# Kernel optimization log

Measured on AMD Instinct MI355X. Metric: run time of the kernel, lower is better.

The kernel has to match this reference:

```python
import jax, jax.numpy as jnp
import numpy as np

NUM_LAYERS = 4
HIDDEN = 512
HEADS = 8
DK = HIDDEN // HEADS
REPR_IN = 53
REPR_HID = 32
LN_EPS = 1e-5


def _mask_by_1dmask(x, mask):
    # x: [B,H,L,L], mask: [B,L] bool
    pair = mask[:, :, None] & mask[:, None, :]          # [B,L,L]
    masked = jnp.where(pair[:, None, :, :], x, -jnp.inf)
    all_inf = jnp.all(masked == -jnp.inf, axis=-1, keepdims=True)
    return jnp.where(all_inf, 0.0, masked)


def _layernorm(x, g, b):
    mu = jnp.mean(x, axis=-1, keepdims=True)
    var = jnp.mean((x - mu) ** 2, axis=-1, keepdims=True)
    return (x - mu) * jax.lax.rsqrt(var + LN_EPS) * g + b


def _attn_block(x, mask, refCov, Wq, bq, Wk, bk, Wv, bv, Wo, bo,
                Wr1, br1, Wr2, br2, ln_g, ln_b):
    B, L, h = x.shape
    residual = x
    q = (x @ Wq + bq).reshape(B, L, HEADS, DK).transpose(0, 2, 1, 3)  # [B,H,L,dk]
    k = (x @ Wk + bk).reshape(B, L, HEADS, DK).transpose(0, 2, 1, 3)
    v = (x @ Wv + bv).reshape(B, L, HEADS, DK).transpose(0, 2, 1, 3)
    scores = jnp.einsum('bhid,bhjd->bhij', q, k) / np.sqrt(DK).astype(np.float32)
    scores = _mask_by_1dmask(scores, mask)
    attn_w = jax.nn.softmax(scores, axis=-1)
    # per-pair MLP bias: [B,L,L,53] -> [B,L,L,H] -> [B,H,L,L]
    ref = jax.nn.relu(refCov @ Wr1 + br1) @ Wr2 + br2
    ref = ref.transpose(0, 3, 1, 2)
    ref = _mask_by_1dmask(ref, mask)
    ref_w = jax.nn.softmax(ref, axis=-1)
    comb = attn_w + ref_w
    comb = comb / jnp.sum(comb, axis=-1, keepdims=True)
    out = jnp.einsum('bhij,bhjd->bhid', comb, v)
    out = out.transpose(0, 2, 1, 3).reshape(B, L, h)
    out = out @ Wo + bo
    return _layernorm(residual + out, ln_g, ln_b)


def setup_inputs() -> dict:
    key = jax.random.key(0)
    ks = jax.random.split(key, 20)
    B, L = 8, 384
    s = 0.02
    inp = {
        'x': jax.random.normal(ks[0], (B, L, HIDDEN), jnp.float32),
        'mask': jax.random.randint(ks[1], (B, L), 0, 2) > 0,
        'refCov': jax.random.normal(ks[2], (B, L, L, REPR_IN), jnp.float32),
        'Wq': jax.random.normal(ks[3], (NUM_LAYERS, HIDDEN, HIDDEN)) * s,
        'bq': jnp.zeros((NUM_LAYERS, HIDDEN)),
        'Wk': jax.random.normal(ks[4], (NUM_LAYERS, HIDDEN, HIDDEN)) * s,
        'bk': jnp.zeros((NUM_LAYERS, HIDDEN)),
        'Wv': jax.random.normal(ks[5], (NUM_LAYERS, HIDDEN, HIDDEN)) * s,
        'bv': jnp.zeros((NUM_LAYERS, HIDDEN)),
        'Wo': jax.random.normal(ks[6], (NUM_LAYERS, HIDDEN, HIDDEN)) * s,
        'bo': jnp.zeros((NUM_LAYERS, HIDDEN)),
        'Wr1': jax.random.normal(ks[7], (NUM_LAYERS, REPR_IN, REPR_HID)) * 0.1,
        'br1': jnp.zeros((NUM_LAYERS, REPR_HID)),
        'Wr2': jax.random.normal(ks[8], (NUM_LAYERS, REPR_HID, HEADS)) * 0.1,
        'br2': jnp.zeros((NUM_LAYERS, HEADS)),
        'ln_g': jnp.ones((NUM_LAYERS, HIDDEN)),
        'ln_b': jnp.zeros((NUM_LAYERS, HIDDEN)),
        'fn_g': jnp.ones((HIDDEN,)),
        'fn_b': jnp.zeros((HIDDEN,)),
    }
    return inp


def reference(x, mask, refCov, Wq, bq, Wk, bk, Wv, bv, Wo, bo,
              Wr1, br1, Wr2, br2, ln_g, ln_b, fn_g, fn_b):
    # process_node_feature packs flat nodes into [B,L,h] with zeros at padding;
    # equivalent here to zeroing padded positions of x.
    h = x * mask[:, :, None].astype(x.dtype)
    for i in range(NUM_LAYERS):
        h = _attn_block(h, mask, refCov, Wq[i], bq[i], Wk[i], bk[i],
                        Wv[i], bv[i], Wo[i], bo[i], Wr1[i], br1[i],
                        Wr2[i], br2[i], ln_g[i], ln_b[i])
    h = _layernorm(h, fn_g, fn_b)
    return jnp.sum(h * mask[:, :, None].astype(h.dtype), axis=1)  # [B, HIDDEN]
```

## Files before the change

kernel.cpp:

```cpp
#include <hip/hip_runtime.h>
#include <hip/hip_bf16.h>
#include <cstdint>

constexpr int LSEQ  = 384;
constexpr int BATCH = 8;
constexpr int HID   = 512;
constexpr int NHEAD = 8;
constexpr int DKH   = 64;
constexpr int NLAY  = 4;
constexpr int BL    = BATCH * LSEQ;
constexpr int LL2   = LSEQ * LSEQ;
constexpr int BH    = BATCH * NHEAD;

typedef __bf16 bf16x8 __attribute__((ext_vector_type(8)));
typedef float  f32x4  __attribute__((ext_vector_type(4)));
typedef unsigned short ushort_t;

__device__ inline bf16x8 load_frag(const void* p) {
    uint4 u = *reinterpret_cast<const uint4*>(p);
    return __builtin_bit_cast(bf16x8, u);
}
__device__ inline bf16x8 zero_frag() {
    uint4 u = {0u, 0u, 0u, 0u};
    return __builtin_bit_cast(bf16x8, u);
}
__device__ inline f32x4 mfma16(bf16x8 a, bf16x8 b, f32x4 c) {
    return __builtin_amdgcn_mfma_f32_16x16x32_bf16(a, b, c, 0, 0, 0);
}
__device__ inline float b2f(__hip_bfloat16 v) { return __bfloat162float(v); }
__device__ inline ushort_t bfbits(float f) {
    __hip_bfloat16 b = __float2bfloat16(f);
    return *(ushort_t*)&b;
}

__global__ __launch_bounds__(1024) void mask_norm_kernel(
    const unsigned char* __restrict__ raw, unsigned char* __restrict__ m)
{
    __shared__ int fl;
    const int tid = threadIdx.x;
    if (tid == 0) fl = 0;
    __syncthreads();
    int f = 0;
    for (int i = tid; i < BL; i += 1024) {
        const unsigned char v = raw[i];
        if (v > 1) f |= 1;
        if (v && (i & 3)) f |= 2;
        if (v && ((i & 7) == 4)) f |= 4;
        if (v && ((i & 3) <= 1)) f |= 8;
    }
    if (f) atomicOr(&fl, f);
    __syncthreads();
    const int ff = fl;
    int stride, off;
    if (ff & 1) { if (ff & 8) { stride = 2; off = 0; } else { stride = 4; off = 2; } }
    else if (ff & 2) { stride = 1; off = 0; }
    else if (ff & 4) { stride = 4; off = 0; }
    else             { stride = 8; off = 0; }
    for (int i = tid; i < BL; i += 1024)
        m[i] = raw[(size_t)i * stride + off] ? 1 : 0;
}

__global__ __launch_bounds__(256) void wconv_kernel(
    const float* __restrict__ Wq, const float* __restrict__ Wk,
    const float* __restrict__ Wv, const float* __restrict__ Wo,
    ushort_t* __restrict__ WTqkv, ushort_t* __restrict__ WTo)
{
    __shared__ float tile[32][33];
    const int t = blockIdx.x;
    const int ml = t >> 8;
    const int rest = t & 255;
    const int mi = ml >> 2, l = ml & 3;
    const int tk = (rest & 15) * 32;
    const int tn = (rest >> 4) * 32;
    const float* W = (mi == 0) ? Wq : (mi == 1) ? Wk : (mi == 2) ? Wv : Wo;
    const float* src = W + (size_t)l * HID * HID;
    const int c = threadIdx.x & 31, r = threadIdx.x >> 5;
    for (int rr = r; rr < 32; rr += 8)
        tile[rr][c] = src[(size_t)(tk + rr) * HID + tn + c];
    __syncthreads();
    ushort_t* dst = (mi < 3)
        ? WTqkv + ((size_t)l * 1536 + mi * 512) * HID
        : WTo   + (size_t)l * HID * HID;
    for (int rr = r; rr < 32; rr += 8)
        dst[(size_t)(tn + rr) * HID + tk + c] = bfbits(tile[c][rr]);
}

__global__ __launch_bounds__(256) void refw_kernel(
    const float* __restrict__ Wr1, const float* __restrict__ Wr2,
    ushort_t* __restrict__ W1T, ushort_t* __restrict__ W2T)
{
    const int tid = blockIdx.x * 256 + threadIdx.x;
    if (tid < 4 * 32 * 64) {
        const int l = tid >> 11, rem = tid & 2047;
        const int n = rem >> 6, k = rem & 63;
        W1T[tid] = (k < 53) ? bfbits(Wr1[(l * 53 + k) * 32 + n]) : (ushort_t)0;
    } else if (tid < 4 * 32 * 64 + 4 * 16 * 32) {
        const int t2 = tid - 8192;
        const int l = t2 >> 9, rem = t2 & 511;
        const int n = rem >> 5, k = rem & 31;
        W2T[t2] = (n < 8) ? bfbits(Wr2[(l * 32 + k) * 8 + n]) : (ushort_t)0;
    }
}

__global__ __launch_bounds__(256) void pack_kernel(
    const float* __restrict__ x, const unsigned char* __restrict__ mask,
    float* __restrict__ h, __hip_bfloat16* __restrict__ hb)
{
    const int idx = blockIdx.x * 256 + threadIdx.x;
    const int row = idx >> 9;
    const float v = mask[row] ? x[idx] : 0.f;
    h[idx] = v;
    hb[idx] = __float2bfloat16(v);
}

__global__ __launch_bounds__(256) void refmlp_kernel(
    const float* __restrict__ refCov,
    const ushort_t* __restrict__ W1T, const float* __restrict__ br1,
    const ushort_t* __restrict__ W2T, const float* __restrict__ br2,
    __hip_bfloat16* __restrict__ refL)
{
    __shared__ ushort_t smem[256 * 56];

    const int tid = threadIdx.x;
    const int w = tid >> 6, lane = tid & 63;
    const int lr = lane & 15, quad = lane >> 4;
    const size_t p0 = (size_t)blockIdx.x * 256;
    const int b = (int)(p0 / LL2);
    const int rem0 = (int)(p0 - (size_t)b * LL2);

    const float4* src4 = reinterpret_cast<const float4*>(refCov + p0 * 53);
    for (int f = tid; f < 3392; f += 256) {
        float4 v = src4[f];
        const int e = f * 4;
        #pragma unroll
        for (int k = 0; k < 4; ++k) {
            const int g = e + k;
            const int row = g / 53;
            const int col = g - row * 53;
            smem[row * 56 + col] = bfbits(((const float*)&v)[k]);
        }
    }
    smem[tid * 56 + 53] = 0;
    smem[tid * 56 + 54] = 0;
    smem[tid * 56 + 55] = 0;
    __syncthreads();

    bf16x8 afr[4][2];
    #pragma unroll
    for (int mi = 0; mi < 4; ++mi) {
        const ushort_t* rp = smem + (w * 64 + mi * 16 + lr) * 56;
        afr[mi][0] = load_frag(rp + quad * 8);
        afr[mi][1] = (quad < 3) ? load_frag(rp + 32 + quad * 8) : zero_frag();
    }
    __syncthreads();

    ushort_t* C1w = smem + w * 2560;

    #pragma unroll
    for (int l = 0; l < NLAY; ++l) {
        const float bias0 = br1[l * 32 + lr];
        const float bias1 = br1[l * 32 + 16 + lr];
        const float bias2 = br2[l * 8 + (lr & 7)];
        bf16x8 w1f[2][2];
        #pragma unroll
        for (int ni = 0; ni < 2; ++ni)
            #pragma unroll
            for (int ks = 0; ks < 2; ++ks)
                w1f[ni][ks] = load_frag(W1T + ((l * 32 + ni * 16 + lr) * 64) + ks * 32 + quad * 8);
        bf16x8 w2f = load_frag(W2T + (l * 16 + lr) * 32 + quad * 8);

        f32x4 acc[4][2];
        #pragma unroll
        for (int mi = 0; mi < 4; ++mi) {
            acc[mi][0] = (f32x4){bias0, bias0, bias0, bias0};
            acc[mi][1] = (f32x4){bias1, bias1, bias1, bias1};
        }
        #pragma unroll
        for (int mi = 0; mi < 4; ++mi) {
            acc[mi][0] = mfma16(afr[mi][0], w1f[0][0], acc[mi][0]);
            acc[mi][0] = mfma16(afr[mi][1], w1f[0][1], acc[mi][0]);
            acc[mi][1] = mfma16(afr[mi][0], w1f[1][0], acc[mi][1]);
            acc[mi][1] = mfma16(afr[mi][1], w1f[1][1], acc[mi][1]);
        }
        #pragma unroll
        for (int mi = 0; mi < 4; ++mi)
            #pragma unroll
            for (int ni = 0; ni < 2; ++ni)
                #pragma unroll
                for (int r = 0; r < 4; ++r)
                    C1w[(mi * 16 + quad * 4 + r) * 40 + ni * 16 + lr] =
                        bfbits(fmaxf(acc[mi][ni][r], 0.f));

        #pragma unroll
        for (int mi = 0; mi < 4; ++mi) {
            bf16x8 a2 = load_frag(C1w + (mi * 16 + lr) * 40 + quad * 8);
            f32x4 a = (f32x4){bias2, bias2, bias2, bias2};
            a = mfma16(a2, w2f, a);
            if (lr < 8) {
                uint2 pk;
                pk.x = (unsigned)bfbits(a[0]) | ((unsigned)bfbits(a[1]) << 16);
                pk.y = (unsigned)bfbits(a[2]) | ((unsigned)bfbits(a[3]) << 16);
                const size_t plane = ((size_t)(l * 8 + b) * 8 + lr) * LL2;
                *reinterpret_cast<uint2*>((ushort_t*)refL + plane + rem0 +
                                          w * 64 + mi * 16 + quad * 4) = pk;
            }
        }
    }
}

__global__ __launch_bounds__(256) void gemm_qkv_kernel(
    const __hip_bfloat16* __restrict__ A,
    const __hip_bfloat16* __restrict__ BT,
    const float* __restrict__ bq, const float* __restrict__ bk,
    const float* __restrict__ bv,
    __hip_bfloat16* __restrict__ q, __hip_bfloat16* __restrict__ kk,
    __hip_bfloat16* __restrict__ vT)
{
    const int bm = blockIdx.x % (BL / 64);
    const int bn = blockIdx.x / (BL / 64);
    const int wv = threadIdx.x >> 6;
    const int lane = threadIdx.x & 63;
    const int lr = lane & 15, quad = lane >> 4;
    const int m0 = bm * 64 + (wv & 1) * 32;
    const int n0g = bn * 64 + (wv >> 1) * 32;
    f32x4 acc[2][2];
    #pragma unroll
    for (int i = 0; i < 2; ++i)
        #pragma unroll
        for (int j = 0; j < 2; ++j) acc[i][j] = (f32x4){0.f, 0.f, 0.f, 0.f};
    const __hip_bfloat16* a0p = A + (size_t)(m0 + lr) * HID;
    const __hip_bfloat16* a1p = A + (size_t)(m0 + 16 + lr) * HID;
    const __hip_bfloat16* b0p = BT + (size_t)(n0g + lr) * HID;
    const __hip_bfloat16* b1p = BT + (size_t)(n0g + 16 + lr) * HID;
    #pragma unroll 4
    for (int k0 = 0; k0 < HID; k0 += 32) {
        const int ka = k0 + quad * 8;
        bf16x8 a0 = load_frag(a0p + ka);
        bf16x8 a1 = load_frag(a1p + ka);
        bf16x8 b0 = load_frag(b0p + ka);
        bf16x8 b1 = load_frag(b1p + ka);
        acc[0][0] = mfma16(a0, b0, acc[0][0]);
        acc[0][1] = mfma16(a0, b1, acc[0][1]);
        acc[1][0] = mfma16(a1, b0, acc[1][0]);
        acc[1][1] = mfma16(a1, b1, acc[1][1]);
    }
    const int mat = n0g >> 9;
    const float* bias = (mat == 0) ? bq : (mat == 1) ? bk : bv;
    const float scale = (mat == 0) ? 0.125f : 1.0f;
    __hip_bfloat16* outp = (mat == 0) ? q : (mat == 1) ? kk : vT;
    #pragma unroll
    for (int mi = 0; mi < 2; ++mi)
        #pragma unroll
        for (int ni = 0; ni < 2; ++ni)
            #pragma unroll
            for (int r = 0; r < 4; ++r) {
                const int m = m0 + mi * 16 + quad * 4 + r;
                const int ng = n0g + ni * 16 + lr;
                const int n = ng & 511;
                float v = (acc[mi][ni][r] + bias[n]) * scale;
                const int bb = m / LSEQ, ii = m % LSEQ;
                const int hh = n >> 6, d = n & 63;
                if (mat == 2)
                    outp[((size_t)(bb * NHEAD + hh) * DKH + d) * LSEQ + ii] = __float2bfloat16(v);
                else
                    outp[((size_t)(bb * NHEAD + hh) * LSEQ + ii) * DKH + d] = __float2bfloat16(v);
            }
}

__global__ __launch_bounds__(256) void gemm_oproj_kernel(
    const __hip_bfloat16* __restrict__ A,
    const __hip_bfloat16* __restrict__ BT,
    const float* __restrict__ bias,
    float* __restrict__ outf)
{
    const int bm = blockIdx.x % (BL / 64);
    const int bn = blockIdx.x / (BL / 64);
    const int wv = threadIdx.x >> 6;
    const int lane = threadIdx.x & 63;
    const int lr = lane & 15, quad = lane >> 4;
    const int m0 = bm * 64 + (wv & 1) * 32;
    const int n0 = bn * 64 + (wv >> 1) * 32;
    f32x4 acc[2][2];
    #pragma unroll
    for (int i = 0; i < 2; ++i)
        #pragma unroll
        for (int j = 0; j < 2; ++j) acc[i][j] = (f32x4){0.f, 0.f, 0.f, 0.f};
    const __hip_bfloat16* a0p = A + (size_t)(m0 + lr) * HID;
    const __hip_bfloat16* a1p = A + (size_t)(m0 + 16 + lr) * HID;
    const __hip_bfloat16* b0p = BT + (size_t)(n0 + lr) * HID;
    const __hip_bfloat16* b1p = BT + (size_t)(n0 + 16 + lr) * HID;
    #pragma unroll 4
    for (int k0 = 0; k0 < HID; k0 += 32) {
        const int ka = k0 + quad * 8;
        bf16x8 a0 = load_frag(a0p + ka);
        bf16x8 a1 = load_frag(a1p + ka);
        bf16x8 b0 = load_frag(b0p + ka);
        bf16x8 b1 = load_frag(b1p + ka);
        acc[0][0] = mfma16(a0, b0, acc[0][0]);
        acc[0][1] = mfma16(a0, b1, acc[0][1]);
        acc[1][0] = mfma16(a1, b0, acc[1][0]);
        acc[1][1] = mfma16(a1, b1, acc[1][1]);
    }
    #pragma unroll
    for (int mi = 0; mi < 2; ++mi)
        #pragma unroll
        for (int ni = 0; ni < 2; ++ni)
            #pragma unroll
            for (int r = 0; r < 4; ++r) {
                const int m = m0 + mi * 16 + quad * 4 + r;
                const int n = n0 + ni * 16 + lr;
                outf[(size_t)m * HID + n] = acc[mi][ni][r] + bias[n];
            }
}

__global__ __launch_bounds__(256) void gemm_scores_kernel(
    const __hip_bfloat16* __restrict__ Q,
    const __hip_bfloat16* __restrict__ Km,
    float* __restrict__ S)
{
    const int bh = blockIdx.x / 36;
    const int t = blockIdx.x % 36;
    const int bm = t % 6, bn = t / 6;
    const int wv = threadIdx.x >> 6;
    const int lane = threadIdx.x & 63;
    const int lr = lane & 15, quad = lane >> 4;
    const int m0 = bm * 64 + (wv & 1) * 32;
    const int n0 = bn * 64 + (wv >> 1) * 32;
    const __hip_bfloat16* qb = Q + (size_t)bh * LSEQ * DKH;
    const __hip_bfloat16* kb = Km + (size_t)bh * LSEQ * DKH;
    f32x4 acc[2][2];
    #pragma unroll
    for (int i = 0; i < 2; ++i)
        #pragma unroll
        for (int j = 0; j < 2; ++j) acc[i][j] = (f32x4){0.f, 0.f, 0.f, 0.f};
    #pragma unroll
    for (int k0 = 0; k0 < DKH; k0 += 32) {
        const int ka = k0 + quad * 8;
        bf16x8 a0 = load_frag(qb + (size_t)(m0 + lr) * DKH + ka);
        bf16x8 a1 = load_frag(qb + (size_t)(m0 + 16 + lr) * DKH + ka);
        bf16x8 b0 = load_frag(kb + (size_t)(n0 + lr) * DKH + ka);
        bf16x8 b1 = load_frag(kb + (size_t)(n0 + 16 + lr) * DKH + ka);
        acc[0][0] = mfma16(a0, b0, acc[0][0]);
        acc[0][1] = mfma16(a0, b1, acc[0][1]);
        acc[1][0] = mfma16(a1, b0, acc[1][0]);
        acc[1][1] = mfma16(a1, b1, acc[1][1]);
    }
    float* srow = S + (size_t)bh * LL2;
    #pragma unroll
    for (int mi = 0; mi < 2; ++mi)
        #pragma unroll
        for (int ni = 0; ni < 2; ++ni)
            #pragma unroll
            for (int r = 0; r < 4; ++r) {
                const int m = m0 + mi * 16 + quad * 4 + r;
                const int n = n0 + ni * 16 + lr;
                srow[(size_t)m * LSEQ + n] = acc[mi][ni][r];
            }
}

__global__ __launch_bounds__(256) void softmax_comb_kernel(
    const float* __restrict__ S, const __hip_bfloat16* __restrict__ refl,
    const unsigned char* __restrict__ mask, __hip_bfloat16* __restrict__ comb)
{
    const int wv = threadIdx.x >> 6, lane = threadIdx.x & 63;
    const int row = blockIdx.x * 4 + wv;
    const int bh = row / LSEQ, i = row % LSEQ;
    const int b = bh >> 3;
    const size_t roff = (size_t)row * LSEQ;
    __hip_bfloat16* crow = comb + roff;
    if (!mask[b * LSEQ + i]) {
        const __hip_bfloat16 z = __float2bfloat16(0.f);
        #pragma unroll
        for (int t = 0; t < 6; ++t) crow[lane + 64 * t] = z;
        return;
    }
    const float* srow = S + roff;
    const __hip_bfloat16* rrow = refl + roff;
    float sv[6], rv[6];
    #pragma unroll
    for (int t = 0; t < 6; ++t) {
        const int j = lane + 64 * t;
        const bool vm = mask[b * LSEQ + j] != 0;
        sv[t] = vm ? srow[j] : -1e30f;
        rv[t] = vm ? b2f(rrow[j]) : -1e30f;
    }
    float ms = -1e30f, mr = -1e30f;
    #pragma unroll
    for (int t = 0; t < 6; ++t) { ms = fmaxf(ms, sv[t]); mr = fmaxf(mr, rv[t]); }
    #pragma unroll
    for (int off = 32; off > 0; off >>= 1) {
        ms = fmaxf(ms, __shfl_xor(ms, off));
        mr = fmaxf(mr, __shfl_xor(mr, off));
    }
    float es[6], er[6], Ss = 0.f, Sr = 0.f;
    #pragma unroll
    for (int t = 0; t < 6; ++t) {
        es[t] = __expf(sv[t] - ms); Ss += es[t];
        er[t] = __expf(rv[t] - mr); Sr += er[t];
    }
    #pragma unroll
    for (int off = 32; off > 0; off >>= 1) {
        Ss += __shfl_xor(Ss, off);
        Sr += __shfl_xor(Sr, off);
    }
    const float cs = 0.5f / Ss, cr = 0.5f / Sr;
    #pragma unroll
    for (int t = 0; t < 6; ++t)
        crow[lane + 64 * t] = __float2bfloat16(es[t] * cs + er[t] * cr);
}

__global__ __launch_bounds__(256) void gemm_out_kernel(
    const __hip_bfloat16* __restrict__ C,
    const __hip_bfloat16* __restrict__ VT,
    __hip_bfloat16* __restrict__ AO)
{
    const int bh = blockIdx.x / 6;
    const int bm = blockIdx.x % 6;
    const int wv = threadIdx.x >> 6;
    const int lane = threadIdx.x & 63;
    const int lr = lane & 15, quad = lane >> 4;
    const int m0 = bm * 64 + (wv & 1) * 32;
    const int n0 = (wv >> 1) * 32;
    const __hip_bfloat16* cb = C + (size_t)bh * LL2;
    const __hip_bfloat16* vb = VT + (size_t)bh * DKH * LSEQ;
    f32x4 acc[2][2];
    #pragma unroll
    for (int i = 0; i < 2; ++i)
        #pragma unroll
        for (int j = 0; j < 2; ++j) acc[i][j] = (f32x4){0.f, 0.f, 0.f, 0.f};
    #pragma unroll 4
    for (int k0 = 0; k0 < LSEQ; k0 += 32) {
        const int ka = k0 + quad * 8;
        bf16x8 a0 = load_frag(cb + (size_t)(m0 + lr) * LSEQ + ka);
        bf16x8 a1 = load_frag(cb + (size_t)(m0 + 16 + lr) * LSEQ + ka);
        bf16x8 b0 = load_frag(vb + (size_t)(n0 + lr) * LSEQ + ka);
        bf16x8 b1 = load_frag(vb + (size_t)(n0 + 16 + lr) * LSEQ + ka);
        acc[0][0] = mfma16(a0, b0, acc[0][0]);
        acc[0][1] = mfma16(a0, b1, acc[0][1]);
        acc[1][0] = mfma16(a1, b0, acc[1][0]);
        acc[1][1] = mfma16(a1, b1, acc[1][1]);
    }
    const int bb = bh >> 3, hh = bh & 7;
    #pragma unroll
    for (int mi = 0; mi < 2; ++mi)
        #pragma unroll
        for (int ni = 0; ni < 2; ++ni)
            #pragma unroll
            for (int r = 0; r < 4; ++r) {
                const int m = m0 + mi * 16 + quad * 4 + r;
                const int n = n0 + ni * 16 + lr;
                AO[(size_t)(bb * LSEQ + m) * HID + hh * DKH + n] =
                    __float2bfloat16(acc[mi][ni][r]);
            }
}

__global__ __launch_bounds__(256) void ln_kernel(
    const float* __restrict__ resid, const float* __restrict__ proj,
    const float* __restrict__ g, const float* __restrict__ beta,
    float* __restrict__ outf, __hip_bfloat16* __restrict__ outb,
    const unsigned char* __restrict__ mask, int flags)
{
    const int row = blockIdx.x, tid = threadIdx.x;
    const size_t base = (size_t)row * HID;
    float x0 = resid[base + tid], x1 = resid[base + tid + 256];
    if (flags & 1) { x0 += proj[base + tid]; x1 += proj[base + tid + 256]; }
    float s = x0 + x1, s2 = x0 * x0 + x1 * x1;
    #pragma unroll
    for (int off = 32; off > 0; off >>= 1) {
        s += __shfl_xor(s, off);
        s2 += __shfl_xor(s2, off);
    }
    __shared__ float rs[4], rs2[4];
    if ((tid & 63) == 0) { rs[tid >> 6] = s; rs2[tid >> 6] = s2; }
    __syncthreads();
    s = rs[0] + rs[1] + rs[2] + rs[3];
    s2 = rs2[0] + rs2[1] + rs2[2] + rs2[3];
    const float mu = s * (1.f / HID);
    const float var = s2 * (1.f / HID) - mu * mu;
    const float rstd = rsqrtf(var + 1e-5f);
    float y0 = (x0 - mu) * rstd * g[tid] + beta[tid];
    float y1 = (x1 - mu) * rstd * g[tid + 256] + beta[tid + 256];
    if ((flags & 2) && !mask[row]) { y0 = 0.f; y1 = 0.f; }
    outf[base + tid] = y0;
    outf[base + tid + 256] = y1;
    if (flags & 4) {
        outb[base + tid] = __float2bfloat16(y0);
        outb[base + tid + 256] = __float2bfloat16(y1);
    }
}

__global__ __launch_bounds__(512) void reduce_kernel(
    const float* __restrict__ hf, float* __restrict__ out)
{
    const int b = blockIdx.x, c = threadIdx.x;
    float s = 0.f;
    for (int i = 0; i < LSEQ; ++i)
        s += hf[((size_t)(b * LSEQ + i)) * HID + c];
    out[b * HID + c] = s;
}

extern "C" void kernel_launch(void* const* d_in, const int* in_sizes, int n_in,
                              void* d_out, int out_size, void* d_ws, size_t ws_size,
                              hipStream_t stream)
{
    const float* x   = (const float*)d_in[0];
    const unsigned char* mraw = (const unsigned char*)d_in[1];
    const float* refCov = (const float*)d_in[2];
    const float* Wq = (const float*)d_in[3];
    const float* bq = (const float*)d_in[4];
    const float* Wk = (const float*)d_in[5];
    const float* bk = (const float*)d_in[6];
    const float* Wv = (const float*)d_in[7];
    const float* bv = (const float*)d_in[8];
    const float* Wo = (const float*)d_in[9];
    const float* bo = (const float*)d_in[10];
    const float* Wr1 = (const float*)d_in[11];
    const float* br1 = (const float*)d_in[12];
    const float* Wr2 = (const float*)d_in[13];
    const float* br2 = (const float*)d_in[14];
    const float* ln_g = (const float*)d_in[15];
    const float* ln_b = (const float*)d_in[16];
    const float* fn_g = (const float*)d_in[17];
    const float* fn_b = (const float*)d_in[18];
    float* outp = (float*)d_out;

    char* ws = (char*)d_ws;
    size_t off = 0;
    auto alloc = [&](size_t bytes) -> char* {
        char* p = ws + off;
        off += (bytes + 255) & ~(size_t)255;
        return p;
    };
    __hip_bfloat16* refL  = (__hip_bfloat16*)alloc((size_t)NLAY * BH * LL2 * 2);
    float*          h     = (float*)alloc((size_t)BL * HID * 4);
    __hip_bfloat16* hb    = (__hip_bfloat16*)alloc((size_t)BL * HID * 2);
    __hip_bfloat16* q     = (__hip_bfloat16*)alloc((size_t)BH * LSEQ * DKH * 2);
    __hip_bfloat16* kk    = (__hip_bfloat16*)alloc((size_t)BH * LSEQ * DKH * 2);
    __hip_bfloat16* vT    = (__hip_bfloat16*)alloc((size_t)BH * DKH * LSEQ * 2);
    float*          S     = (float*)alloc((size_t)BH * LL2 * 4);
    __hip_bfloat16* comb  = (__hip_bfloat16*)alloc((size_t)BH * LL2 * 2);
    __hip_bfloat16* AO    = (__hip_bfloat16*)alloc((size_t)BL * HID * 2);
    float*          proj  = (float*)alloc((size_t)BL * HID * 4);
    ushort_t*       WTqkv = (ushort_t*)alloc((size_t)NLAY * 1536 * HID * 2);
    ushort_t*       WTo   = (ushort_t*)alloc((size_t)NLAY * HID * HID * 2);
    ushort_t*       W1T   = (ushort_t*)alloc((size_t)4 * 32 * 64 * 2);
    ushort_t*       W2T   = (ushort_t*)alloc((size_t)4 * 16 * 32 * 2);
    unsigned char*  msk   = (unsigned char*)alloc(BL);
    float*          hfin  = S;

    mask_norm_kernel<<<1, 1024, 0, stream>>>(mraw, msk);
    wconv_kernel<<<4096, 256, 0, stream>>>(Wq, Wk, Wv, Wo, WTqkv, WTo);
    refw_kernel<<<40, 256, 0, stream>>>(Wr1, Wr2, W1T, W2T);
    pack_kernel<<<6144, 256, 0, stream>>>(x, msk, h, hb);
    refmlp_kernel<<<4608, 256, 0, stream>>>(refCov, W1T, br1, W2T, br2, refL);

    for (int l = 0; l < NLAY; ++l) {
        const __hip_bfloat16* WTl = (const __hip_bfloat16*)(WTqkv + (size_t)l * 1536 * HID);
        const __hip_bfloat16* WTol = (const __hip_bfloat16*)(WTo + (size_t)l * HID * HID);
        gemm_qkv_kernel<<<1152, 256, 0, stream>>>(hb, WTl, bq + l * HID, bk + l * HID,
                                                  bv + l * HID, q, kk, vT);
        gemm_scores_kernel<<<2304, 256, 0, stream>>>(q, kk, S);
        softmax_comb_kernel<<<6144, 256, 0, stream>>>(S, refL + (size_t)l * BH * LL2, msk, comb);
        gemm_out_kernel<<<384, 256, 0, stream>>>(comb, vT, AO);
        gemm_oproj_kernel<<<384, 256, 0, stream>>>(AO, WTol, bo + l * HID, proj);
        ln_kernel<<<3072, 256, 0, stream>>>(h, proj, ln_g + l * HID, ln_b + l * HID,
                                            h, hb, nullptr, 1 | 4);
    }
    ln_kernel<<<3072, 256, 0, stream>>>(h, nullptr, fn_g, fn_b, hfin, nullptr, msk, 2);
    reduce_kernel<<<8, 512, 0, stream>>>(hfin, outp);
}
```

Baseline: 907.6 us.

## Fuse scores, dual softmax and PV matmul into one attention kernel

Replaces the three per-layer kernels (QK^T scores to fp32 global, softmax combine to bf16 global, comb@V) with one kernel per 32-row tile of each batch-head. Scores are kept in registers, the row max and sum are reduced across wavefronts through shared memory, and the combined probabilities are written to LDS and fed straight into the PV MFMA. This removes the round trips of the full fp32 scores and bf16 comb tensors through HBM plus two launches per layer. The cost is more registers per thread, a 25KB LDS tile, and only 768 blocks, which may lower occupancy.

```diff
diff --git a/kernel.cpp b/kernel.cpp
--- a/kernel.cpp
+++ b/kernel.cpp
@@ -313,145 +313,149 @@
             }
 }
 
-__global__ __launch_bounds__(256) void gemm_scores_kernel(
+__global__ __launch_bounds__(256) void attn_fused_kernel(
     const __hip_bfloat16* __restrict__ Q,
     const __hip_bfloat16* __restrict__ Km,
-    float* __restrict__ S)
-{
-    const int bh = blockIdx.x / 36;
-    const int t = blockIdx.x % 36;
-    const int bm = t % 6, bn = t / 6;
-    const int wv = threadIdx.x >> 6;
-    const int lane = threadIdx.x & 63;
+    const __hip_bfloat16* __restrict__ VT,
+    const __hip_bfloat16* __restrict__ refl,
+    const unsigned char* __restrict__ mask,
+    __hip_bfloat16* __restrict__ AO)
+{
+    __shared__ __align__(16) ushort_t Pl[32 * 392];
+    __shared__ float redm_s[2][2][16], redm_r[2][2][16];
+    __shared__ float reds_s[2][2][16], reds_r[2][2][16];
+
+    const int bh = blockIdx.x / 12;
+    const int i0 = (blockIdx.x % 12) * 32;
+    const int b  = bh >> 3, hh = bh & 7;
+    const int w = threadIdx.x >> 6, lane = threadIdx.x & 63;
+    const int s = w & 1, h2 = w >> 1;
     const int lr = lane & 15, quad = lane >> 4;
-    const int m0 = bm * 64 + (wv & 1) * 32;
-    const int n0 = bn * 64 + (wv >> 1) * 32;
-    const __hip_bfloat16* qb = Q + (size_t)bh * LSEQ * DKH;
+
+    const __hip_bfloat16* qb = Q  + (size_t)bh * LSEQ * DKH;
     const __hip_bfloat16* kb = Km + (size_t)bh * LSEQ * DKH;
-    f32x4 acc[2][2];
-    #pragma unroll
-    for (int i = 0; i < 2; ++i)
-        #pragma unroll
-        for (int j = 0; j < 2; ++j) acc[i][j] = (f32x4){0.f, 0.f, 0.f, 0.f};
+    const unsigned char* mrow = mask + b * LSEQ;
+
+    f32x4 acc[12];
+    #pragma unroll
+    for (int nt = 0; nt < 12; ++nt) acc[nt] = (f32x4){0.f, 0.f, 0.f, 0.f};
     #pragma unroll
     for (int k0 = 0; k0 < DKH; k0 += 32) {
         const int ka = k0 + quad * 8;
-        bf16x8 a0 = load_frag(qb + (size_t)(m0 + lr) * DKH + ka);
-        bf16x8 a1 = load_frag(qb + (size_t)(m0 + 16 + lr) * DKH + ka);
-        bf16x8 b0 = load_frag(kb + (size_t)(n0 + lr) * DKH + ka);
-        bf16x8 b1 = load_frag(kb + (size_t)(n0 + 16 + lr) * DKH + ka);
-        acc[0][0] = mfma16(a0, b0, acc[0][0]);
-        acc[0][1] = mfma16(a0, b1, acc[0][1]);
-        acc[1][0] = mfma16(a1, b0, acc[1][0]);
-        acc[1][1] = mfma16(a1, b1, acc[1][1]);
-    }
-    float* srow = S + (size_t)bh * LL2;
-    #pragma unroll
-    for (int mi = 0; mi < 2; ++mi)
-        #pragma unroll
-        for (int ni = 0; ni < 2; ++ni)
-            #pragma unroll
-            for (int r = 0; r < 4; ++r) {
-                const int m = m0 + mi * 16 + quad * 4 + r;
-                const int n = n0 + ni * 16 + lr;
-                srow[(size_t)m * LSEQ + n] = acc[mi][ni][r];
-            }
-}
-
-__global__ __launch_bounds__(256) void softmax_comb_kernel(
-    const float* __restrict__ S, const __hip_bfloat16* __restrict__ refl,
-    const unsigned char* __restrict__ mask, __hip_bfloat16* __restrict__ comb)
-{
-    const int wv = threadIdx.x >> 6, lane = threadIdx.x & 63;
-    const int row = blockIdx.x * 4 + wv;
-    const int bh = row / LSEQ, i = row % LSEQ;
-    const int b = bh >> 3;
-    const size_t roff = (size_t)row * LSEQ;
-    __hip_bfloat16* crow = comb + roff;
-    if (!mask[b * LSEQ + i]) {
-        const __hip_bfloat16 z = __float2bfloat16(0.f);
-        #pragma unroll
-        for (int t = 0; t < 6; ++t) crow[lane + 64 * t] = z;
-        return;
-    }
-    const float* srow = S + roff;
-    const __hip_bfloat16* rrow = refl + roff;
-    float sv[6], rv[6];
-    #pragma unroll
-    for (int t = 0; t < 6; ++t) {
-        const int j = lane + 64 * t;
-        const bool vm = mask[b * LSEQ + j] != 0;
-        sv[t] = vm ? srow[j] : -1e30f;
-        rv[t] = vm ? b2f(rrow[j]) : -1e30f;
-    }
-    float ms = -1e30f, mr = -1e30f;
-    #pragma unroll
-    for (int t = 0; t < 6; ++t) { ms = fmaxf(ms, sv[t]); mr = fmaxf(mr, rv[t]); }
-    #pragma unroll
-    for (int off = 32; off > 0; off >>= 1) {
-        ms = fmaxf(ms, __shfl_xor(ms, off));
-        mr = fmaxf(mr, __shfl_xor(mr, off));
-    }
-    float es[6], er[6], Ss = 0.f, Sr = 0.f;
-    #pragma unroll
-    for (int t = 0; t < 6; ++t) {
-        es[t] = __expf(sv[t] - ms); Ss += es[t];
-        er[t] = __expf(rv[t] - mr); Sr += er[t];
-    }
-    #pragma unroll
-    for (int off = 32; off > 0; off >>= 1) {
-        Ss += __shfl_xor(Ss, off);
-        Sr += __shfl_xor(Sr, off);
-    }
-    const float cs = 0.5f / Ss, cr = 0.5f / Sr;
-    #pragma unroll
-    for (int t = 0; t < 6; ++t)
-        crow[lane + 64 * t] = __float2bfloat16(es[t] * cs + er[t] * cr);
-}
-
-__global__ __launch_bounds__(256) void gemm_out_kernel(
-    const __hip_bfloat16* __restrict__ C,
-    const __hip_bfloat16* __restrict__ VT,
-    __hip_bfloat16* __restrict__ AO)
-{
-    const int bh = blockIdx.x / 6;
-    const int bm = blockIdx.x % 6;
-    const int wv = threadIdx.x >> 6;
-    const int lane = threadIdx.x & 63;
-    const int lr = lane & 15, quad = lane >> 4;
-    const int m0 = bm * 64 + (wv & 1) * 32;
-    const int n0 = (wv >> 1) * 32;
-    const __hip_bfloat16* cb = C + (size_t)bh * LL2;
+        bf16x8 a = load_frag(qb + (size_t)(i0 + s * 16 + lr) * DKH + ka);
+        #pragma unroll
+        for (int nt = 0; nt < 12; ++nt) {
+            bf16x8 bf = load_frag(kb + (size_t)(h2 * 192 + nt * 16 + lr) * DKH + ka);
+            acc[nt] = mfma16(a, bf, acc[nt]);
+        }
+    }
+
+    bool vm[12];
+    #pragma unroll
+    for (int nt = 0; nt < 12; ++nt)
+        vm[nt] = mrow[h2 * 192 + nt * 16 + lr] != 0;
+
+    const __hip_bfloat16* rbase = refl + (size_t)bh * LL2 +
+                                  (size_t)(i0 + s * 16) * LSEQ + h2 * 192;
+    float rv[12][4];
+    #pragma unroll
+    for (int nt = 0; nt < 12; ++nt)
+        #pragma unroll
+        for (int r = 0; r < 4; ++r)
+            rv[nt][r] = b2f(rbase[(size_t)(quad * 4 + r) * LSEQ + nt * 16 + lr]);
+
+    float ms[4], mr2[4];
+    #pragma unroll
+    for (int r = 0; r < 4; ++r) { ms[r] = -1e30f; mr2[r] = -1e30f; }
+    #pragma unroll
+    for (int nt = 0; nt < 12; ++nt)
+        #pragma unroll
+        for (int r = 0; r < 4; ++r) {
+            acc[nt][r] = vm[nt] ? acc[nt][r] : -1e30f;
+            rv[nt][r]  = vm[nt] ? rv[nt][r]  : -1e30f;
+            ms[r]  = fmaxf(ms[r],  acc[nt][r]);
+            mr2[r] = fmaxf(mr2[r], rv[nt][r]);
+        }
+    #pragma unroll
+    for (int off = 8; off > 0; off >>= 1)
+        #pragma unroll
+        for (int r = 0; r < 4; ++r) {
+            ms[r]  = fmaxf(ms[r],  __shfl_xor(ms[r],  off));
+            mr2[r] = fmaxf(mr2[r], __shfl_xor(mr2[r], off));
+        }
+    if (lr == 0)
+        #pragma unroll
+        for (int r = 0; r < 4; ++r) {
+            redm_s[s][h2][quad * 4 + r] = ms[r];
+            redm_r[s][h2][quad * 4 + r] = mr2[r];
+        }
+    __syncthreads();
+    #pragma unroll
+    for (int r = 0; r < 4; ++r) {
+        ms[r]  = fmaxf(redm_s[s][0][quad * 4 + r], redm_s[s][1][quad * 4 + r]);
+        mr2[r] = fmaxf(redm_r[s][0][quad * 4 + r], redm_r[s][1][quad * 4 + r]);
+    }
+
+    float Ss[4] = {0.f, 0.f, 0.f, 0.f}, Sr[4] = {0.f, 0.f, 0.f, 0.f};
+    #pragma unroll
+    for (int nt = 0; nt < 12; ++nt)
+        #pragma unroll
+        for (int r = 0; r < 4; ++r) {
+            acc[nt][r] = __expf(acc[nt][r] - ms[r]);  Ss[r] += acc[nt][r];
+            rv[nt][r]  = __expf(rv[nt][r]  - mr2[r]); Sr[r] += rv[nt][r];
+        }
+    #pragma unroll
+    for (int off = 8; off > 0; off >>= 1)
+        #pragma unroll
+        for (int r = 0; r < 4; ++r) {
+            Ss[r] += __shfl_xor(Ss[r], off);
+            Sr[r] += __shfl_xor(Sr[r], off);
+        }
+    if (lr == 0)
+        #pragma unroll
+        for (int r = 0; r < 4; ++r) {
+            reds_s[s][h2][quad * 4 + r] = Ss[r];
+            reds_r[s][h2][quad * 4 + r] = Sr[r];
+        }
+    __syncthreads();
+
+    float cs[4], cr[4], rm[4];
+    #pragma unroll
+    for (int r = 0; r < 4; ++r) {
+        const float SsF = reds_s[s][0][quad * 4 + r] + reds_s[s][1][quad * 4 + r];
+        const float SrF = reds_r[s][0][quad * 4 + r] + reds_r[s][1][quad * 4 + r];
+        cs[r] = 0.5f / SsF;
+        cr[r] = 0.5f / SrF;
+        rm[r] = mrow[i0 + s * 16 + quad * 4 + r] ? 1.f : 0.f;
+    }
+    #pragma unroll
+    for (int nt = 0; nt < 12; ++nt)
+        #pragma unroll
+        for (int r = 0; r < 4; ++r)
+            Pl[(s * 16 + quad * 4 + r) * 392 + h2 * 192 + nt * 16 + lr] =
+                bfbits((acc[nt][r] * cs[r] + rv[nt][r] * cr[r]) * rm[r]);
+    __syncthreads();
+
     const __hip_bfloat16* vb = VT + (size_t)bh * DKH * LSEQ;
-    f32x4 acc[2][2];
-    #pragma unroll
-    for (int i = 0; i < 2; ++i)
-        #pragma unroll
-        for (int j = 0; j < 2; ++j) acc[i][j] = (f32x4){0.f, 0.f, 0.f, 0.f};
+    f32x4 oa[2];
+    oa[0] = (f32x4){0.f, 0.f, 0.f, 0.f};
+    oa[1] = (f32x4){0.f, 0.f, 0.f, 0.f};
     #pragma unroll 4
     for (int k0 = 0; k0 < LSEQ; k0 += 32) {
         const int ka = k0 + quad * 8;
-        bf16x8 a0 = load_frag(cb + (size_t)(m0 + lr) * LSEQ + ka);
-        bf16x8 a1 = load_frag(cb + (size_t)(m0 + 16 + lr) * LSEQ + ka);
-        bf16x8 b0 = load_frag(vb + (size_t)(n0 + lr) * LSEQ + ka);
-        bf16x8 b1 = load_frag(vb + (size_t)(n0 + 16 + lr) * LSEQ + ka);
-        acc[0][0] = mfma16(a0, b0, acc[0][0]);
-        acc[0][1] = mfma16(a0, b1, acc[0][1]);
-        acc[1][0] = mfma16(a1, b0, acc[1][0]);
-        acc[1][1] = mfma16(a1, b1, acc[1][1]);
-    }
-    const int bb = bh >> 3, hh = bh & 7;
-    #pragma unroll
-    for (int mi = 0; mi < 2; ++mi)
-        #pragma unroll
-        for (int ni = 0; ni < 2; ++ni)
-            #pragma unroll
-            for (int r = 0; r < 4; ++r) {
-                const int m = m0 + mi * 16 + quad * 4 + r;
-                const int n = n0 + ni * 16 + lr;
-                AO[(size_t)(bb * LSEQ + m) * HID + hh * DKH + n] =
-                    __float2bfloat16(acc[mi][ni][r]);
-            }
+        bf16x8 a = load_frag(Pl + (s * 16 + lr) * 392 + ka);
+        #pragma unroll
+        for (int dt = 0; dt < 2; ++dt) {
+            bf16x8 bf = load_frag(vb + (size_t)(h2 * 32 + dt * 16 + lr) * LSEQ + ka);
+            oa[dt] = mfma16(a, bf, oa[dt]);
+        }
+    }
+    #pragma unroll
+    for (int dt = 0; dt < 2; ++dt)
+        #pragma unroll
+        for (int r = 0; r < 4; ++r)
+            AO[(size_t)(b * LSEQ + i0 + s * 16 + quad * 4 + r) * HID +
+               hh * DKH + h2 * 32 + dt * 16 + lr] = __float2bfloat16(oa[dt][r]);
 }
 
 __global__ __launch_bounds__(256) void ln_kernel(
@@ -538,7 +542,6 @@
     __hip_bfloat16* kk    = (__hip_bfloat16*)alloc((size_t)BH * LSEQ * DKH * 2);
     __hip_bfloat16* vT    = (__hip_bfloat16*)alloc((size_t)BH * DKH * LSEQ * 2);
     float*          S     = (float*)alloc((size_t)BH * LL2 * 4);
-    __hip_bfloat16* comb  = (__hip_bfloat16*)alloc((size_t)BH * LL2 * 2);
     __hip_bfloat16* AO    = (__hip_bfloat16*)alloc((size_t)BL * HID * 2);
     float*          proj  = (float*)alloc((size_t)BL * HID * 4);
     ushort_t*       WTqkv = (ushort_t*)alloc((size_t)NLAY * 1536 * HID * 2);
@@ -559,9 +562,8 @@
         const __hip_bfloat16* WTol = (const __hip_bfloat16*)(WTo + (size_t)l * HID * HID);
         gemm_qkv_kernel<<<1152, 256, 0, stream>>>(hb, WTl, bq + l * HID, bk + l * HID,
                                                   bv + l * HID, q, kk, vT);
-        gemm_scores_kernel<<<2304, 256, 0, stream>>>(q, kk, S);
-        softmax_comb_kernel<<<6144, 256, 0, stream>>>(S, refL + (size_t)l * BH * LL2, msk, comb);
-        gemm_out_kernel<<<384, 256, 0, stream>>>(comb, vT, AO);
+        attn_fused_kernel<<<768, 256, 0, stream>>>(q, kk, vT,
+                                                   refL + (size_t)l * BH * LL2, msk, AO);
         gemm_oproj_kernel<<<384, 256, 0, stream>>>(AO, WTol, bo + l * HID, proj);
         ln_kernel<<<3072, 256, 0, stream>>>(h, proj, ln_g + l * HID, ln_b + l * HID,
                                             h, hb, nullptr, 1 | 4);
```

Result: faster. 840.2 us (-7.4%).
